# Kernel tuning notes

Hardware: AMD Instinct MI355X
Metric: run time of the kernel (lower is better)

Reference implementation:

```python
import jax, jax.numpy as jnp
import numpy as np
from jax import lax

BOOST_STRENGTH = 0.5
WEIGHT_DENSITY = 0.05


def setup_inputs() -> dict:
    key = jax.random.key(0)
    k1, k2, k3, k4, k5 = jax.random.split(key, 5)
    batch, d_in, d_out = 16384, 512, 4096
    x = jax.random.normal(k1, (batch, d_in), dtype=jnp.float32)
    W = jax.random.normal(k2, (d_out, d_in), dtype=jnp.float32) * 0.05
    b = jax.random.normal(k3, (d_out,), dtype=jnp.float32) * 0.01
    w_mask = (jax.random.uniform(k4, (d_out, d_in)) < WEIGHT_DENSITY).astype(jnp.float32)
    # duty cycle buffer in [0, 0.1]
    duty_cycle = jax.random.uniform(k5, (d_out,), dtype=jnp.float32) * 0.1
    k = 205  # round(0.05 * 4096)
    return {"x": x, "W": W, "b": b, "w_mask": w_mask,
            "duty_cycle": duty_cycle, "k": k}


def reference(x, W, b, w_mask, duty_cycle, k):
    # SparseWeights: masked dense linear
    y = x @ (W * w_mask).T + b                      # [B, n]
    n = y.shape[-1]
    target_density = k / n
    # KWinners boosting: exp of duty-cycle deficit
    boost = jnp.exp(BOOST_STRENGTH * (target_density - duty_cycle))  # [n]
    boosted = y * boost                              # [B, n]
    # top-k threshold per row on boosted values
    thresh = lax.top_k(boosted, k)[0][..., -1:]      # [B, 1]
    # mask: keep ORIGINAL activations at winner positions
    return jnp.where(boosted >= thresh, y, 0.0)
```

## Files before the change

### kernel.cpp

```cpp
#include <hip/hip_runtime.h>
#include <stdint.h>
#include <math.h>


#define BATCH 16384
#define K_DIM 512
#define N_DIM 4096
#define RPB 4
#define MAXE 64

typedef float f32x4 __attribute__((ext_vector_type(4)));
typedef unsigned int u32;

__global__ void boost_kernel(const float* __restrict__ duty,
                             const int* __restrict__ kptr,
                             float* __restrict__ boost, int* __restrict__ Emax) {
  const int j = blockIdx.x * blockDim.x + threadIdx.x;
  if (j == 0) Emax[0] = 0;
  if (j < N_DIM) {
    const float td = (float)((double)kptr[0] / (double)N_DIM);
    const float arg = 0.5f * (td - duty[j]);
    boost[j] = (float)exp((double)arg);
  }
}

__global__ __launch_bounds__(256) void compress_kernel(
    const float* __restrict__ W, const float* __restrict__ mask,
    unsigned short* __restrict__ cIdx, float* __restrict__ cVal,
    int* __restrict__ cnt, int* __restrict__ Emax) {
  const int j = blockIdx.x * 4 + (threadIdx.x >> 6);
  const int lane = threadIdx.x & 63;
  if (j >= N_DIM) return;
  const float* mr = mask + (size_t)j * K_DIM;
  const float* wr = W + (size_t)j * K_DIM;
  int base = 0;
#pragma unroll
  for (int c = 0; c < K_DIM / 64; ++c) {
    const int k = c * 64 + lane;
    const bool act = (mr[k] != 0.0f);
    const unsigned long long bal = __ballot(act);
    const int pos = __popcll(bal & ((1ull << lane) - 1ull));
    if (act && base + pos < MAXE) {
      cIdx[(size_t)j * MAXE + base + pos] = (unsigned short)k;
      cVal[(size_t)j * MAXE + base + pos] = wr[k];
    }
    base += (int)__popcll(bal);
  }
  if (lane == 0) {
    const int c = base < MAXE ? base : MAXE;
    cnt[j] = c;
    atomicMax(Emax, c);
  }
}

__global__ __launch_bounds__(256) void fill_kernel(
    const unsigned short* __restrict__ cIdx, const float* __restrict__ cVal,
    const int* __restrict__ cnt, uint2* __restrict__ pairT) {
  const int j = blockIdx.x * 256 + threadIdx.x;
  const int c = cnt[j];
#pragma unroll 4
  for (int e = 0; e < MAXE; ++e) {
    uint2 pr;
    if (e < c) {
      pr.x = (u32)cIdx[(size_t)j * MAXE + e] * 16u;
      pr.y = __float_as_uint(cVal[(size_t)j * MAXE + e]);
    } else {
      pr.x = 0u; pr.y = 0u;
    }
    pairT[(size_t)e * N_DIM + j] = pr;
  }
}

__global__ __launch_bounds__(256) void fused_kernel(
    const float* __restrict__ x, const float* __restrict__ bvec,
    const uint2* __restrict__ pairT, const float* __restrict__ boost,
    const int* __restrict__ Emax, const int* __restrict__ kptr,
    float* __restrict__ out) {
  __shared__ __align__(16) float sxT[K_DIM][RPB];
  __shared__ u32 hist[256];
  __shared__ u32 s_prefix, s_kk;

  const int tid = threadIdx.x;
  const int row0 = blockIdx.x * RPB;

  for (int i = tid; i < K_DIM; i += 256)
#pragma unroll
    for (int r = 0; r < RPB; ++r)
      sxT[i][r] = x[(size_t)(row0 + r) * K_DIM + i];

  const int E = Emax[0];
  const int kk0 = kptr[0];
  float a[RPB][16];
#pragma unroll
  for (int r = 0; r < RPB; ++r)
#pragma unroll
    for (int u = 0; u < 16; ++u) a[r][u] = 0.0f;
  __syncthreads();

  for (int e = 0; e < E; ++e) {
    const uint2* pe = pairT + (size_t)e * N_DIM + tid;
#pragma unroll
    for (int u = 0; u < 16; ++u) {
      const uint2 pr = pe[u * 256];
      const f32x4 xs = *(const f32x4*)((const char*)&sxT[0][0] + pr.x);
      const float w = __uint_as_float(pr.y);
      a[0][u] = fmaf(w, xs[0], a[0][u]);
      a[1][u] = fmaf(w, xs[1], a[1][u]);
      a[2][u] = fmaf(w, xs[2], a[2][u]);
      a[3][u] = fmaf(w, xs[3], a[3][u]);
    }
  }

  float y[RPB][16], bl[16];
#pragma unroll
  for (int u = 0; u < 16; ++u) {
    const int j = u * 256 + tid;
    const float bj = bvec[j];
    bl[u] = boost[j];
#pragma unroll
    for (int r = 0; r < RPB; ++r) y[r][u] = a[r][u] + bj;
  }

#pragma unroll 1
  for (int r = 0; r < RPB; ++r) {
    u32 key[16];
#pragma unroll
    for (int u = 0; u < 16; ++u) {
      const float t = y[r][u] * bl[u];
      const u32 v = __float_as_uint(t);
      key[u] = (v & 0x80000000u) ? ~v : (v | 0x80000000u);
    }
    if (tid == 0) { s_prefix = 0u; s_kk = (u32)kk0; }
    __syncthreads();

#pragma unroll 1
    for (int round = 0; round < 4; ++round) {
      const int shift = 24 - 8 * round;
      const u32 prefix = s_prefix;
      const u32 kk = s_kk;
      const u32 himask = round ? (0xFFFFFFFFu << (32 - 8 * round)) : 0u;
      hist[tid] = 0u;
      __syncthreads();
#pragma unroll
      for (int u = 0; u < 16; ++u)
        if ((key[u] & himask) == prefix)
          atomicAdd(&hist[(key[u] >> shift) & 255u], 1u);
      __syncthreads();
      if (tid < 64) {
        const int l = tid;
        const u32 h0 = hist[l * 4], h1 = hist[l * 4 + 1];
        const u32 h2 = hist[l * 4 + 2], h3 = hist[l * 4 + 3];
        const u32 s3 = h3, s2 = h2 + s3, s1 = h1 + s2, s0 = h0 + s1;
        u32 t = s0;
#pragma unroll
        for (int off = 1; off < 64; off <<= 1) {
          const u32 v = __shfl_down(t, off, 64);
          if (l + off < 64) t += v;
        }
        const u32 Eab = t - s0;
        const u32 S0 = Eab + s0, S1 = Eab + s1, S2 = Eab + s2, S3 = Eab + s3;
        const u32 S[5] = {S0, S1, S2, S3, Eab};
#pragma unroll
        for (int i = 0; i < 4; ++i)
          if (S[i] >= kk && S[i + 1] < kk) {
            s_prefix = prefix | ((u32)(l * 4 + i) << shift);
            s_kk = kk - S[i + 1];
          }
      }
      __syncthreads();
    }
    const u32 tkey = s_prefix;

    float* orow = out + (size_t)(row0 + r) * N_DIM;
#pragma unroll
    for (int u = 0; u < 16; ++u)
      orow[u * 256 + tid] = (key[u] >= tkey) ? y[r][u] : 0.0f;
    __syncthreads();
  }
}

extern "C" void kernel_launch(void* const* d_in, const int* in_sizes, int n_in,
                              void* d_out, int out_size, void* d_ws, size_t ws_size,
                              hipStream_t stream) {
  const float* x     = (const float*)d_in[0];
  const float* W     = (const float*)d_in[1];
  const float* bvec  = (const float*)d_in[2];
  const float* wmask = (const float*)d_in[3];
  const float* duty  = (const float*)d_in[4];
  const int* kptr    = (const int*)d_in[5];
  float* out = (float*)d_out;

  uint8_t* ws = (uint8_t*)d_ws;
  unsigned short* cIdx = (unsigned short*)(ws);
  float* cVal          = (float*)(ws + (1u << 20));
  int* cnt             = (int*)(ws + (2u << 20));
  float* boost         = (float*)(ws + (2u << 20) + (64u << 10));
  int* Emax            = (int*)(ws + (2u << 20) + (128u << 10));
  uint2* pairT         = (uint2*)(ws + (4u << 20));

  boost_kernel<<<16, 256, 0, stream>>>(duty, kptr, boost, Emax);
  compress_kernel<<<N_DIM / 4, 256, 0, stream>>>(W, wmask, cIdx, cVal, cnt, Emax);
  fill_kernel<<<N_DIM / 256, 256, 0, stream>>>(cIdx, cVal, cnt, pairT);
  fused_kernel<<<BATCH / RPB, 256, 0, stream>>>(x, bvec, pairT, boost, Emax,
                                                kptr, out);
}
```

Measured before the change: 849.8 us.

## Sort output columns by nonzero count to cut padded sparse iterations

Adds a single-block counting sort that orders output neurons by their per-row nonzero count, then assigns the sorted columns to threads so each thread's 16 columns have similar counts. Each thread loops only to the maximum count of its own columns instead of the global maximum, which removes most of the zero-padded FMA work. The partial sums are then scattered back to original column order through shared memory before the top-k selection. This costs an extra kernel launch, a permutation table, and a shared-memory scatter with extra barriers per row.

```diff
diff --git a/kernel.cpp b/kernel.cpp
--- a/kernel.cpp
+++ b/kernel.cpp
@@ -14,9 +14,8 @@
 
 __global__ void boost_kernel(const float* __restrict__ duty,
                              const int* __restrict__ kptr,
-                             float* __restrict__ boost, int* __restrict__ Emax) {
+                             float* __restrict__ boost) {
   const int j = blockIdx.x * blockDim.x + threadIdx.x;
-  if (j == 0) Emax[0] = 0;
   if (j < N_DIM) {
     const float td = (float)((double)kptr[0] / (double)N_DIM);
     const float arg = 0.5f * (td - duty[j]);
@@ -27,7 +26,7 @@
 __global__ __launch_bounds__(256) void compress_kernel(
     const float* __restrict__ W, const float* __restrict__ mask,
     unsigned short* __restrict__ cIdx, float* __restrict__ cVal,
-    int* __restrict__ cnt, int* __restrict__ Emax) {
+    int* __restrict__ cnt) {
   const int j = blockIdx.x * 4 + (threadIdx.x >> 6);
   const int lane = threadIdx.x & 63;
   if (j >= N_DIM) return;
@@ -46,18 +45,40 @@
     }
     base += (int)__popcll(bal);
   }
-  if (lane == 0) {
-    const int c = base < MAXE ? base : MAXE;
-    cnt[j] = c;
-    atomicMax(Emax, c);
-  }
+  if (lane == 0) cnt[j] = base < MAXE ? base : MAXE;
+}
+
+__global__ __launch_bounds__(256) void sort_kernel(
+    const int* __restrict__ cnt, int* __restrict__ perm, int* __restrict__ tE) {
+  __shared__ int hist[MAXE + 1];
+  __shared__ int off[MAXE + 1];
+  const int tid = threadIdx.x;
+  if (tid <= MAXE) hist[tid] = 0;
+  __syncthreads();
+  for (int j = tid; j < N_DIM; j += 256) atomicAdd(&hist[cnt[j]], 1);
+  __syncthreads();
+  if (tid == 0) {
+    int s = 0;
+    for (int c = 0; c <= MAXE; ++c) { off[c] = s; s += hist[c]; }
+  }
+  __syncthreads();
+  for (int j = tid; j < N_DIM; j += 256) {
+    const int p = atomicAdd(&off[cnt[j]], 1);
+    perm[p] = j;
+  }
+  __syncthreads();
+  tE[tid] = cnt[perm[tid * 16 + 15]];
 }
 
 __global__ __launch_bounds__(256) void fill_kernel(
     const unsigned short* __restrict__ cIdx, const float* __restrict__ cVal,
-    const int* __restrict__ cnt, uint2* __restrict__ pairT) {
-  const int j = blockIdx.x * 256 + threadIdx.x;
+    const int* __restrict__ cnt, const int* __restrict__ perm,
+    uint2* __restrict__ pairT, int* __restrict__ orig) {
+  const int s = blockIdx.x * 256 + threadIdx.x;
+  const int j = perm[s];
   const int c = cnt[j];
+  const int slot = (s & 15) * 256 + (s >> 4);
+  orig[slot] = j;
 #pragma unroll 4
   for (int e = 0; e < MAXE; ++e) {
     uint2 pr;
@@ -67,16 +88,16 @@
     } else {
       pr.x = 0u; pr.y = 0u;
     }
-    pairT[(size_t)e * N_DIM + j] = pr;
+    pairT[(size_t)e * N_DIM + slot] = pr;
   }
 }
 
 __global__ __launch_bounds__(256) void fused_kernel(
     const float* __restrict__ x, const float* __restrict__ bvec,
     const uint2* __restrict__ pairT, const float* __restrict__ boost,
-    const int* __restrict__ Emax, const int* __restrict__ kptr,
-    float* __restrict__ out) {
-  __shared__ __align__(16) float sxT[K_DIM][RPB];
+    const int* __restrict__ orig, const int* __restrict__ tE,
+    const int* __restrict__ kptr, float* __restrict__ out) {
+  __shared__ __align__(16) float smem[N_DIM];
   __shared__ u32 hist[256];
   __shared__ u32 s_prefix, s_kk;
 
@@ -86,9 +107,9 @@
   for (int i = tid; i < K_DIM; i += 256)
 #pragma unroll
     for (int r = 0; r < RPB; ++r)
-      sxT[i][r] = x[(size_t)(row0 + r) * K_DIM + i];
-
-  const int E = Emax[0];
+      smem[i * 4 + r] = x[(size_t)(row0 + r) * K_DIM + i];
+
+  const int myE = tE[tid];
   const int kk0 = kptr[0];
   float a[RPB][16];
 #pragma unroll
@@ -97,12 +118,12 @@
     for (int u = 0; u < 16; ++u) a[r][u] = 0.0f;
   __syncthreads();
 
-  for (int e = 0; e < E; ++e) {
+  for (int e = 0; e < myE; ++e) {
     const uint2* pe = pairT + (size_t)e * N_DIM + tid;
 #pragma unroll
     for (int u = 0; u < 16; ++u) {
       const uint2 pr = pe[u * 256];
-      const f32x4 xs = *(const f32x4*)((const char*)&sxT[0][0] + pr.x);
+      const f32x4 xs = *(const f32x4*)((const char*)smem + pr.x);
       const float w = __uint_as_float(pr.y);
       a[0][u] = fmaf(w, xs[0], a[0][u]);
       a[1][u] = fmaf(w, xs[1], a[1][u]);
@@ -111,27 +132,26 @@
     }
   }
 
-  float y[RPB][16], bl[16];
-#pragma unroll
-  for (int u = 0; u < 16; ++u) {
-    const int j = u * 256 + tid;
-    const float bj = bvec[j];
-    bl[u] = boost[j];
-#pragma unroll
-    for (int r = 0; r < RPB; ++r) y[r][u] = a[r][u] + bj;
-  }
-
 #pragma unroll 1
   for (int r = 0; r < RPB; ++r) {
+    __syncthreads();
+#pragma unroll
+    for (int u = 0; u < 16; ++u)
+      smem[orig[u * 256 + tid]] = a[r][u];
+    if (tid == 0) { s_prefix = 0u; s_kk = (u32)kk0; }
+    __syncthreads();
+
+    float y[16], bl[16];
     u32 key[16];
 #pragma unroll
     for (int u = 0; u < 16; ++u) {
-      const float t = y[r][u] * bl[u];
+      const int j = u * 256 + tid;
+      y[u] = smem[j] + bvec[j];
+      bl[u] = boost[j];
+      const float t = y[u] * bl[u];
       const u32 v = __float_as_uint(t);
       key[u] = (v & 0x80000000u) ? ~v : (v | 0x80000000u);
     }
-    if (tid == 0) { s_prefix = 0u; s_kk = (u32)kk0; }
-    __syncthreads();
 
 #pragma unroll 1
     for (int round = 0; round < 4; ++round) {
@@ -158,8 +178,7 @@
           if (l + off < 64) t += v;
         }
         const u32 Eab = t - s0;
-        const u32 S0 = Eab + s0, S1 = Eab + s1, S2 = Eab + s2, S3 = Eab + s3;
-        const u32 S[5] = {S0, S1, S2, S3, Eab};
+        const u32 S[5] = {Eab + s0, Eab + s1, Eab + s2, Eab + s3, Eab};
 #pragma unroll
         for (int i = 0; i < 4; ++i)
           if (S[i] >= kk && S[i + 1] < kk) {
@@ -174,8 +193,7 @@
     float* orow = out + (size_t)(row0 + r) * N_DIM;
 #pragma unroll
     for (int u = 0; u < 16; ++u)
-      orow[u * 256 + tid] = (key[u] >= tkey) ? y[r][u] : 0.0f;
-    __syncthreads();
+      orow[u * 256 + tid] = (key[u] >= tkey) ? y[u] : 0.0f;
   }
 }
 
@@ -195,12 +213,15 @@
   float* cVal          = (float*)(ws + (1u << 20));
   int* cnt             = (int*)(ws + (2u << 20));
   float* boost         = (float*)(ws + (2u << 20) + (64u << 10));
-  int* Emax            = (int*)(ws + (2u << 20) + (128u << 10));
+  int* perm            = (int*)(ws + (2u << 20) + (128u << 10));
+  int* tE              = (int*)(ws + (2u << 20) + (192u << 10));
+  int* orig            = (int*)(ws + (2u << 20) + (256u << 10));
   uint2* pairT         = (uint2*)(ws + (4u << 20));
 
-  boost_kernel<<<16, 256, 0, stream>>>(duty, kptr, boost, Emax);
-  compress_kernel<<<N_DIM / 4, 256, 0, stream>>>(W, wmask, cIdx, cVal, cnt, Emax);
-  fill_kernel<<<N_DIM / 256, 256, 0, stream>>>(cIdx, cVal, cnt, pairT);
-  fused_kernel<<<BATCH / RPB, 256, 0, stream>>>(x, bvec, pairT, boost, Emax,
+  boost_kernel<<<16, 256, 0, stream>>>(duty, kptr, boost);
+  compress_kernel<<<N_DIM / 4, 256, 0, stream>>>(W, wmask, cIdx, cVal, cnt);
+  sort_kernel<<<1, 256, 0, stream>>>(cnt, perm, tE);
+  fill_kernel<<<N_DIM / 256, 256, 0, stream>>>(cIdx, cVal, cnt, perm, pairT, orig);
+  fused_kernel<<<BATCH / RPB, 256, 0, stream>>>(x, bvec, pairT, boost, orig, tE,
                                                 kptr, out);
 }
```

New measurement: 786.5 us. 7.5% less time.
